# Kernel optimization log

Hardware: AMD Instinct MI355X
Metric: run time of the kernel (lower is better)

## Reference

```python
import jax, jax.numpy as jnp
import numpy as np

B, N, D, H = 4, 4096, 128, 8
DH = D // H
EPS = 1e-6


def _layernorm(x, g, b):
    mu = jnp.mean(x, axis=-1, keepdims=True)
    var = jnp.var(x, axis=-1, keepdims=True)
    return (x - mu) * jax.lax.rsqrt(var + EPS) * g + b


def setup_inputs() -> dict:
    key = jax.random.key(0)
    ks = jax.random.split(key, 12)
    p = lambda k, shape: (jax.random.normal(k, shape, jnp.float32) * 0.02)
    x = jax.random.normal(ks[0], (B, N, D), jnp.float32)
    # scale fx so the sigmoid of the N-length contraction is not fully saturated
    fx = jax.random.normal(ks[1], (B, N, D), jnp.float32) / N
    return {
        "x": x,
        "fx": fx,
        "ln1_g": jnp.ones((D,), jnp.float32),
        "ln1_b": jnp.zeros((D,), jnp.float32),
        "wq": p(ks[2], (D, D)),
        "wk": p(ks[3], (D, D)),
        "wv": p(ks[4], (D, D)),
        "wo": p(ks[5], (D, D)),
        "bo": jnp.zeros((D,), jnp.float32),
        "ln2_g": jnp.ones((D,), jnp.float32),
        "ln2_b": jnp.zeros((D,), jnp.float32),
        "w1": p(ks[6], (D, D)),
        "b1": jnp.zeros((D,), jnp.float32),
        "w2": p(ks[7], (D, D)),
        "b2": jnp.zeros((D,), jnp.float32),
    }


def reference(x, fx, ln1_g, ln1_b, wq, wk, wv, wo, bo, ln2_g, ln2_b, w1, b1, w2, b2):
    b, n, d = x.shape
    h, dh = H, d // H
    # --- pre-norm linear self-attention ---
    xn = _layernorm(x, ln1_g, ln1_b)
    def heads(w):  # [b,n,d] @ w^T -> [b,h,n,dh]
        return jnp.einsum('bnd,ed->bne', xn, w).reshape(b, n, h, dh).transpose(0, 2, 1, 3)
    q = jax.nn.softmax(heads(wq), axis=-1)   # softmax over feature dim
    k = jax.nn.softmax(heads(wk), axis=2)    # softmax over sequence dim
    v = heads(wv)
    ctx = jnp.einsum('bhnd,bhne->bhde', k, v)         # [b,h,dh,dh]
    attn = jnp.einsum('bhnd,bhde->bhne', q, ctx)       # [b,h,n,dh]
    attn = attn.transpose(0, 2, 1, 3).reshape(b, n, d)
    attn = jnp.einsum('bnd,ed->bne', attn, wo) + bo
    x = x + attn                                       # residual (dropout=identity)
    # --- pre-norm MLP ---
    y = _layernorm(x, ln2_g, ln2_b)
    y = jax.nn.gelu(jnp.einsum('bnd,ed->bne', y, w1) + b1, approximate=False)
    y = jnp.einsum('bnd,ed->bne', y, w2) + b2
    x = x + y
    # --- quadratic update: sigmoid((x x^T) fx), as written in the module ---
    gram = jnp.einsum('bnd,bmd->bnm', x, x)            # [b,n,n] materialized, faithful
    fx = jax.nn.sigmoid(jnp.einsum('bnm,bmd->bnd', gram, fx))
    return (x, fx)
```

## Files before the change

### kernel.cpp

```cpp
#include <hip/hip_runtime.h>
#include <math.h>

#define BB 4
#define NN 4096
#define DD 128
#define MM (BB*NN)

typedef __attribute__((ext_vector_type(8))) short short8;
typedef __attribute__((ext_vector_type(4))) float f32x4;

__device__ inline short f2bf(float f) {
    unsigned u = __float_as_uint(f);
    u = (u + 0x7FFFu + ((u >> 16) & 1u)) >> 16;
    return (short)u;
}
__device__ inline float bf2f(short s) {
    return __uint_as_float(((unsigned)(unsigned short)s) << 16);
}
__device__ inline short8 pack_bf8(float4 a, float4 b) {
    short8 o;
    o[0] = f2bf(a.x); o[1] = f2bf(a.y); o[2] = f2bf(a.z); o[3] = f2bf(a.w);
    o[4] = f2bf(b.x); o[5] = f2bf(b.y); o[6] = f2bf(b.z); o[7] = f2bf(b.w);
    return o;
}
__device__ inline int swzoff(int row, int col) {
    return ((row * 128 + col) * 2) ^ ((row & 7) << 4);
}

__global__ __launch_bounds__(256) void wprep(const float* __restrict__ w0, const float* __restrict__ w1,
                                             const float* __restrict__ w2, const float* __restrict__ w3,
                                             const float* __restrict__ w4, short* __restrict__ wf) {
    int m = blockIdx.x >> 3;
    int j = (blockIdx.x & 7) * 256 + threadIdx.x;
    const float* W = (m == 0) ? w0 : (m == 1) ? w1 : (m == 2) ? w2 : (m == 3) ? w3 : w4;
    int nt = j >> 8, ks = (j >> 6) & 3, l = j & 63, r = l & 15, g = l >> 4;
    const float* src = W + (size_t)(nt * 16 + r) * DD + 32 * ks + 8 * g;
    float4 a = *(const float4*)src;
    float4 b = *(const float4*)(src + 4);
    ((short8*)(wf + (size_t)m * 16384))[j] = pack_bf8(a, b);
}

__global__ __launch_bounds__(256) void lnctx(const float* __restrict__ x,
                                             const float* __restrict__ lng,
                                             const float* __restrict__ lnb,
                                             const short* __restrict__ wf,
                                             float* __restrict__ partC,
                                             float* __restrict__ pcs) {
    __shared__ float ekL[32][132];
    __shared__ float vL[32][132];
    int t = threadIdx.x;
    int block_row = blockIdx.x * 32;
    int w = t >> 6, l = t & 63, r = l & 15, g = l >> 4;
    int rh = w >> 1, nt0 = (w & 1) << 2;
    int row0 = block_row + rh * 16;

    const float* ap = x + (size_t)(row0 + r) * DD + 8 * g;
    float4 av0[4], av1[4];
    #pragma unroll
    for (int ks = 0; ks < 4; ks++) {
        av0[ks] = *(const float4*)(ap + 32 * ks);
        av1[ks] = *(const float4*)(ap + 32 * ks + 4);
    }
    float s = 0.f, ss = 0.f;
    #pragma unroll
    for (int ks = 0; ks < 4; ks++) {
        float4 a = av0[ks], b = av1[ks];
        s  += a.x + a.y + a.z + a.w + b.x + b.y + b.z + b.w;
        ss += a.x*a.x + a.y*a.y + a.z*a.z + a.w*a.w + b.x*b.x + b.y*b.y + b.z*b.z + b.w*b.w;
    }
    s  += __shfl_xor(s, 16);  s  += __shfl_xor(s, 32);
    ss += __shfl_xor(ss, 16); ss += __shfl_xor(ss, 32);
    float mu = s * (1.0f / DD);
    float var = ss * (1.0f / DD) - mu * mu;
    float rs = rsqrtf(var + 1e-6f);

    short8 af[4];
    #pragma unroll
    for (int ks = 0; ks < 4; ks++) {
        float4 g0 = *(const float4*)(lng + 32 * ks + 8 * g);
        float4 g1 = *(const float4*)(lng + 32 * ks + 8 * g + 4);
        float4 b0 = *(const float4*)(lnb + 32 * ks + 8 * g);
        float4 b1 = *(const float4*)(lnb + 32 * ks + 8 * g + 4);
        float4 n0, n1;
        n0.x = (av0[ks].x - mu) * rs * g0.x + b0.x;
        n0.y = (av0[ks].y - mu) * rs * g0.y + b0.y;
        n0.z = (av0[ks].z - mu) * rs * g0.z + b0.z;
        n0.w = (av0[ks].w - mu) * rs * g0.w + b0.w;
        n1.x = (av1[ks].x - mu) * rs * g1.x + b1.x;
        n1.y = (av1[ks].y - mu) * rs * g1.y + b1.y;
        n1.z = (av1[ks].z - mu) * rs * g1.z + b1.z;
        n1.w = (av1[ks].w - mu) * rs * g1.w + b1.w;
        af[ks] = pack_bf8(n0, n1);
    }

    f32x4 acc[2][4];
    #pragma unroll
    for (int m = 0; m < 2; m++)
        #pragma unroll
        for (int n = 0; n < 4; n++) acc[m][n] = (f32x4){0.f, 0.f, 0.f, 0.f};
    const short8* wp8 = (const short8*)wf;
    #pragma unroll
    for (int ks = 0; ks < 4; ks++)
        #pragma unroll
        for (int m = 0; m < 2; m++)
            #pragma unroll
            for (int n = 0; n < 4; n++)
                acc[m][n] = __builtin_amdgcn_mfma_f32_16x16x32_bf16(
                    af[ks], wp8[(size_t)m * 2048 + ((nt0 + n) * 4 + ks) * 64 + l], acc[m][n], 0, 0, 0);

    #pragma unroll
    for (int n = 0; n < 4; n++) {
        int col = (nt0 + n) * 16 + r;
        #pragma unroll
        for (int j = 0; j < 4; j++) {
            int rowL = rh * 16 + 4 * g + j;
            ekL[rowL][col] = __expf(acc[0][n][j]);
            vL[rowL][col]  = acc[1][n][j];
        }
    }
    __syncthreads();

    int h = t >> 5, sub = t & 31, d = sub >> 1, e0 = (sub & 1) * 8;
    float cs = 0.f;
    float sc[8] = {0.f, 0.f, 0.f, 0.f, 0.f, 0.f, 0.f, 0.f};
    #pragma unroll 8
    for (int row = 0; row < 32; row++) {
        float ekv = ekL[row][h * 16 + d];
        float4 v0 = *(const float4*)&vL[row][h * 16 + e0];
        float4 v1 = *(const float4*)&vL[row][h * 16 + e0 + 4];
        sc[0] += ekv * v0.x; sc[1] += ekv * v0.y; sc[2] += ekv * v0.z; sc[3] += ekv * v0.w;
        sc[4] += ekv * v1.x; sc[5] += ekv * v1.y; sc[6] += ekv * v1.z; sc[7] += ekv * v1.w;
        cs += ekv;
    }
    float* cb = partC + (size_t)blockIdx.x * 2048 + h * 256 + d * 16 + e0;
    *(float4*)cb       = (float4){sc[0], sc[1], sc[2], sc[3]};
    *(float4*)(cb + 4) = (float4){sc[4], sc[5], sc[6], sc[7]};
    if ((sub & 1) == 0) pcs[(size_t)blockIdx.x * 128 + h * 16 + d] = cs;
}

__global__ __launch_bounds__(256) void ctxred(const float* __restrict__ part,
                                              float* __restrict__ ctxacc) {
    int k = blockIdx.x;
    int b = k >> 4, s0 = (k & 15) * 128;
    int t = threadIdx.x;
    int slot = s0 + (t & 127), half = t >> 7;
    float s = 0.f;
    #pragma unroll 8
    for (int c = half * 64; c < half * 64 + 64; c++)
        s += part[(size_t)((b << 7) + c) * 2048 + slot];
    __shared__ float red[128];
    if (half) red[t & 127] = s;
    __syncthreads();
    if (!half) ctxacc[(size_t)b * 2048 + slot] = s + red[t & 127];
}

__global__ __launch_bounds__(256) void build_mt_k(const float* __restrict__ ctxacc,
                                                  const float* __restrict__ pcs,
                                                  const float* __restrict__ wo,
                                                  short* __restrict__ mtfrag) {
    int b = blockIdx.x >> 3, nt = blockIdx.x & 7;
    int t = threadIdx.x;
    __shared__ float ctxL[2048];
    __shared__ float csL[128];
    __shared__ float woL[2048];
    #pragma unroll
    for (int i = 0; i < 8; i++) {
        int idx = i * 256 + t;
        ctxL[idx] = ctxacc[(size_t)b * 2048 + idx];
        woL[idx]  = wo[(size_t)(nt * 16) * DD + idx];
    }
    if (t < 128) {
        float s = 0.f;
        #pragma unroll 8
        for (int c = 0; c < 128; c++) s += pcs[(size_t)(b * 128 + c) * 128 + t];
        csL[t] = s;
    }
    __syncthreads();
    int ks = (t >> 6) & 3, l = t & 63, r = l & 15, g = l >> 4;
    short8 o;
    #pragma unroll
    for (int i2 = 0; i2 < 8; i2++) {
        int k = 32 * ks + 8 * g + i2;
        float inv = 1.0f / csL[k];
        const float* wrow = woL + r * DD + (k >> 4) * 16;
        float s = 0.f;
        #pragma unroll
        for (int eo = 0; eo < 16; eo++) s += ctxL[k * 16 + eo] * wrow[eo];
        o[i2] = f2bf(s * inv);
    }
    ((short8*)(mtfrag + (size_t)b * 16384))[nt * 256 + t] = o;
}

__global__ __launch_bounds__(256) void fused_mid(const float* __restrict__ x,
                                                 const float* __restrict__ ln1g,
                                                 const float* __restrict__ ln1b,
                                                 const short* __restrict__ wqf,
                                                 const short* __restrict__ mtf,
                                                 const float* __restrict__ bo,
                                                 const float* __restrict__ ln2g,
                                                 const float* __restrict__ ln2b,
                                                 const short* __restrict__ w1f,
                                                 const float* __restrict__ b1,
                                                 const short* __restrict__ w2f,
                                                 const float* __restrict__ b2,
                                                 float* __restrict__ xfinal,
                                                 short* __restrict__ xbf) {
    __shared__ __align__(16) char ex[32 * 128 * 2];
    __shared__ float ex2f[32][132];
    __shared__ float redS[4][16], redSS[4][16];
    int t = threadIdx.x;
    int block_row = blockIdx.x * 32;
    int w = t >> 6, l = t & 63, r = l & 15, g = l >> 4;
    int rh = w >> 1, nt0 = (w & 1) << 2;
    int row0 = block_row + rh * 16;
    int rrow = rh * 16 + r;

    const float* ap = x + (size_t)(row0 + r) * DD + 8 * g;
    float4 av0[4], av1[4];
    #pragma unroll
    for (int ks = 0; ks < 4; ks++) {
        av0[ks] = *(const float4*)(ap + 32 * ks);
        av1[ks] = *(const float4*)(ap + 32 * ks + 4);
    }
    if ((w & 1) == 0) {
        #pragma unroll
        for (int ks = 0; ks < 4; ks++) {
            *(float4*)&ex2f[rrow][32 * ks + 8 * g]     = av0[ks];
            *(float4*)&ex2f[rrow][32 * ks + 8 * g + 4] = av1[ks];
        }
    }
    float s = 0.f, ss = 0.f;
    #pragma unroll
    for (int ks = 0; ks < 4; ks++) {
        float4 a = av0[ks], b = av1[ks];
        s  += a.x + a.y + a.z + a.w + b.x + b.y + b.z + b.w;
        ss += a.x*a.x + a.y*a.y + a.z*a.z + a.w*a.w + b.x*b.x + b.y*b.y + b.z*b.z + b.w*b.w;
    }
    s  += __shfl_xor(s, 16);  s  += __shfl_xor(s, 32);
    ss += __shfl_xor(ss, 16); ss += __shfl_xor(ss, 32);
    float mu1 = s * (1.0f / DD);
    float var1 = ss * (1.0f / DD) - mu1 * mu1;
    float rs1 = rsqrtf(var1 + 1e-6f);
    short8 af[4];
    #pragma unroll
    for (int ks = 0; ks < 4; ks++) {
        float4 g0 = *(const float4*)(ln1g + 32 * ks + 8 * g);
        float4 g1 = *(const float4*)(ln1g + 32 * ks + 8 * g + 4);
        float4 b0 = *(const float4*)(ln1b + 32 * ks + 8 * g);
        float4 b1v = *(const float4*)(ln1b + 32 * ks + 8 * g + 4);
        float4 n0, n1;
        n0.x = (av0[ks].x - mu1) * rs1 * g0.x + b0.x;
        n0.y = (av0[ks].y - mu1) * rs1 * g0.y + b0.y;
        n0.z = (av0[ks].z - mu1) * rs1 * g0.z + b0.z;
        n0.w = (av0[ks].w - mu1) * rs1 * g0.w + b0.w;
        n1.x = (av1[ks].x - mu1) * rs1 * g1.x + b1v.x;
        n1.y = (av1[ks].y - mu1) * rs1 * g1.y + b1v.y;
        n1.z = (av1[ks].z - mu1) * rs1 * g1.z + b1v.z;
        n1.w = (av1[ks].w - mu1) * rs1 * g1.w + b1v.w;
        af[ks] = pack_bf8(n0, n1);
    }

    const short8* qp = (const short8*)wqf;
    f32x4 accq[4];
    #pragma unroll
    for (int n = 0; n < 4; n++) accq[n] = (f32x4){0.f, 0.f, 0.f, 0.f};
    #pragma unroll
    for (int ks = 0; ks < 4; ks++)
        #pragma unroll
        for (int n = 0; n < 4; n++)
            accq[n] = __builtin_amdgcn_mfma_f32_16x16x32_bf16(
                af[ks], qp[((nt0 + n) * 4 + ks) * 64 + l], accq[n], 0, 0, 0);
    #pragma unroll
    for (int n = 0; n < 4; n++) {
        int col = (nt0 + n) * 16 + r;
        #pragma unroll
        for (int j = 0; j < 4; j++) {
            float e = __expf(accq[n][j]);
            float sm = e;
            sm += __shfl_xor(sm, 1); sm += __shfl_xor(sm, 2);
            sm += __shfl_xor(sm, 4); sm += __shfl_xor(sm, 8);
            *(short*)(ex + swzoff(rh * 16 + 4 * g + j, col)) = f2bf(e / sm);
        }
    }
    __syncthreads();

    short8 qf[4];
    #pragma unroll
    for (int ks = 0; ks < 4; ks++)
        qf[ks] = *(const short8*)(ex + swzoff(rrow, 32 * ks + 8 * g));
    float xres[4][4];
    #pragma unroll
    for (int n = 0; n < 4; n++)
        #pragma unroll
        for (int j = 0; j < 4; j++)
            xres[n][j] = ex2f[rh * 16 + 4 * g + j][(nt0 + n) * 16 + r];

    const short8* mp = (const short8*)(mtf + (size_t)(block_row >> 12) * 16384);
    f32x4 acc[4];
    #pragma unroll
    for (int n = 0; n < 4; n++) acc[n] = (f32x4){0.f, 0.f, 0.f, 0.f};
    #pragma unroll
    for (int ks = 0; ks < 4; ks++)
        #pragma unroll
        for (int n = 0; n < 4; n++)
            acc[n] = __builtin_amdgcn_mfma_f32_16x16x32_bf16(
                qf[ks], mp[((nt0 + n) * 4 + ks) * 64 + l], acc[n], 0, 0, 0);

    float vv[4][4];
    #pragma unroll
    for (int n = 0; n < 4; n++) {
        int col = (nt0 + n) * 16 + r;
        float bv = bo[col];
        #pragma unroll
        for (int j = 0; j < 4; j++)
            vv[n][j] = acc[n][j] + bv + xres[n][j];
    }

    #pragma unroll
    for (int j = 0; j < 4; j++) {
        float s1  = vv[0][j] + vv[1][j] + vv[2][j] + vv[3][j];
        float s2 = vv[0][j]*vv[0][j] + vv[1][j]*vv[1][j] + vv[2][j]*vv[2][j] + vv[3][j]*vv[3][j];
        s1 += __shfl_xor(s1, 1); s1 += __shfl_xor(s1, 2); s1 += __shfl_xor(s1, 4); s1 += __shfl_xor(s1, 8);
        s2 += __shfl_xor(s2, 1); s2 += __shfl_xor(s2, 2); s2 += __shfl_xor(s2, 4); s2 += __shfl_xor(s2, 8);
        if (r == 0) { redS[w][4 * g + j] = s1; redSS[w][4 * g + j] = s2; }
    }
    __syncthreads();
    int base = w & 2;
    #pragma unroll
    for (int j = 0; j < 4; j++) {
        int rr = 4 * g + j;
        float S  = redS[base][rr]  + redS[base + 1][rr];
        float SS = redSS[base][rr] + redSS[base + 1][rr];
        float mu = S * (1.0f / DD);
        float var = SS * (1.0f / DD) - mu * mu;
        float rs = rsqrtf(var + 1e-6f);
        int rowL = rh * 16 + rr;
        #pragma unroll
        for (int n = 0; n < 4; n++) {
            int col = (nt0 + n) * 16 + r;
            float y = (vv[n][j] - mu) * rs * ln2g[col] + ln2b[col];
            *(short*)(ex + swzoff(rowL, col)) = f2bf(y);
        }
    }
    __syncthreads();
    short8 yf[4];
    #pragma unroll
    for (int ks = 0; ks < 4; ks++)
        yf[ks] = *(const short8*)(ex + swzoff(rrow, 32 * ks + 8 * g));
    __syncthreads();
    const short8* w1p = (const short8*)w1f;
    f32x4 acc2[4];
    #pragma unroll
    for (int n = 0; n < 4; n++) acc2[n] = (f32x4){0.f, 0.f, 0.f, 0.f};
    #pragma unroll
    for (int ks = 0; ks < 4; ks++)
        #pragma unroll
        for (int n = 0; n < 4; n++)
            acc2[n] = __builtin_amdgcn_mfma_f32_16x16x32_bf16(
                yf[ks], w1p[((nt0 + n) * 4 + ks) * 64 + l], acc2[n], 0, 0, 0);
    #pragma unroll
    for (int n = 0; n < 4; n++) {
        int col = (nt0 + n) * 16 + r;
        float bv = b1[col];
        #pragma unroll
        for (int j = 0; j < 4; j++) {
            float v = acc2[n][j] + bv;
            v = 0.5f * v * (1.0f + erff(v * 0.70710678118654752f));
            *(short*)(ex + swzoff(rh * 16 + 4 * g + j, col)) = f2bf(v);
        }
    }
    __syncthreads();
    short8 hf[4];
    #pragma unroll
    for (int ks = 0; ks < 4; ks++)
        hf[ks] = *(const short8*)(ex + swzoff(rrow, 32 * ks + 8 * g));
    const short8* w2p = (const short8*)w2f;
    f32x4 acc3[4];
    #pragma unroll
    for (int n = 0; n < 4; n++) acc3[n] = (f32x4){0.f, 0.f, 0.f, 0.f};
    #pragma unroll
    for (int ks = 0; ks < 4; ks++)
        #pragma unroll
        for (int n = 0; n < 4; n++)
            acc3[n] = __builtin_amdgcn_mfma_f32_16x16x32_bf16(
                hf[ks], w2p[((nt0 + n) * 4 + ks) * 64 + l], acc3[n], 0, 0, 0);
    #pragma unroll
    for (int n = 0; n < 4; n++) {
        int col = (nt0 + n) * 16 + r;
        float bv = b2[col];
        #pragma unroll
        for (int j = 0; j < 4; j++) {
            float v = acc3[n][j] + bv + vv[n][j];
            size_t row = (size_t)(row0 + 4 * g + j);
            xfinal[row * DD + col] = v;
            xbf[row * DD + col] = f2bf(v);
        }
    }
}

__global__ __launch_bounds__(256) void sbuild_p(const short* __restrict__ xf,
                                                const float* __restrict__ fx,
                                                short* __restrict__ part) {
    int b = blockIdx.x >> 6, chunk = blockIdx.x & 63;
    int t = threadIdx.x;
    __shared__ float xs[64 * 128], fs[64 * 128];
    const short* xb = xf + ((size_t)b * NN + chunk * 64) * DD;
    const float* fb = fx + ((size_t)b * NN + chunk * 64) * DD;
    float4* xs4 = (float4*)xs; float4* fs4 = (float4*)fs;
    const short8* xg = (const short8*)xb; const float4* fg = (const float4*)fb;
    #pragma unroll
    for (int i = 0; i < 4; i++) {
        int j = i * 256 + t;
        short8 s8 = xg[j];
        float4 a = {bf2f(s8[0]), bf2f(s8[1]), bf2f(s8[2]), bf2f(s8[3])};
        float4 c = {bf2f(s8[4]), bf2f(s8[5]), bf2f(s8[6]), bf2f(s8[7])};
        xs4[2 * j] = a; xs4[2 * j + 1] = c;
    }
    #pragma unroll
    for (int i = 0; i < 8; i++) {
        int j = i * 256 + t;
        fs4[j] = fg[j];
    }
    __syncthreads();
    int td = t >> 4, te = t & 15;
    float acc[8][8];
    #pragma unroll
    for (int a = 0; a < 8; a++)
        #pragma unroll
        for (int c = 0; c < 8; c++) acc[a][c] = 0.f;
    for (int r = 0; r < 64; r++) {
        float4 x0 = xs4[r * 32 + td * 2], x1 = xs4[r * 32 + td * 2 + 1];
        float4 f0 = fs4[r * 32 + te * 2], f1 = fs4[r * 32 + te * 2 + 1];
        float xv[8] = {x0.x, x0.y, x0.z, x0.w, x1.x, x1.y, x1.z, x1.w};
        float fv[8] = {f0.x, f0.y, f0.z, f0.w, f1.x, f1.y, f1.z, f1.w};
        #pragma unroll
        for (int a = 0; a < 8; a++)
            #pragma unroll
            for (int c = 0; c < 8; c++) acc[a][c] = fmaf(xv[a], fv[c], acc[a][c]);
    }
    short* pb = part + (size_t)blockIdx.x * 16384;
    int d0 = td * 8, e0 = te * 8;
    #pragma unroll
    for (int ei = 0; ei < 8; ei++) {
        short8 o;
        #pragma unroll
        for (int i = 0; i < 8; i++) o[i] = f2bf(acc[i][ei]);
        *(short8*)(pb + (size_t)(e0 + ei) * DD + d0) = o;
    }
}

__global__ __launch_bounds__(256) void sreduce(const short* __restrict__ part,
                                               short* __restrict__ stfrag) {
    int b = blockIdx.x >> 6, grp = blockIdx.x & 63;
    int t = threadIdx.x;
    int slotL = t >> 3, sub = t & 7;
    int j = grp * 32 + slotL;
    int nt = j >> 8, ks = (j >> 6) & 3, l = j & 63, r = l & 15, g = l >> 4;
    int c = nt * 16 + r, k0 = 32 * ks + 8 * g;
    const short* pb = part + (size_t)b * 64 * 16384 + (size_t)c * DD + k0;
    float s[8] = {0.f, 0.f, 0.f, 0.f, 0.f, 0.f, 0.f, 0.f};
    for (int ch = sub; ch < 64; ch += 8) {
        short8 u = *(const short8*)(pb + (size_t)ch * 16384);
        #pragma unroll
        for (int i = 0; i < 8; i++) s[i] += bf2f(u[i]);
    }
    #pragma unroll
    for (int o = 1; o <= 4; o <<= 1)
        #pragma unroll
        for (int i = 0; i < 8; i++) s[i] += __shfl_xor(s[i], o);
    if (sub == 0) {
        short8 o;
        #pragma unroll
        for (int i = 0; i < 8; i++) o[i] = f2bf(s[i]);
        ((short8*)(stfrag + (size_t)b * 16384))[j] = o;
    }
}

__global__ __launch_bounds__(256) void gemm_sig(const short* __restrict__ A,
                                                const short* __restrict__ wfrag,
                                                float* __restrict__ Cf) {
    int t = threadIdx.x;
    int block_row = blockIdx.x * 32;
    int w = t >> 6, l = t & 63, r = l & 15, g = l >> 4;
    int row0 = block_row + ((w >> 1) << 4);
    int nt0 = (w & 1) << 2;
    const short8* ap = (const short8*)(A + (size_t)(row0 + r) * DD + 8 * g);
    short8 af[4];
    #pragma unroll
    for (int ks = 0; ks < 4; ks++) af[ks] = ap[ks * 4];
    const short8* wp8 = (const short8*)(wfrag + (size_t)(block_row >> 12) * 16384);
    f32x4 acc[4];
    #pragma unroll
    for (int n = 0; n < 4; n++) acc[n] = (f32x4){0.f, 0.f, 0.f, 0.f};
    #pragma unroll
    for (int ks = 0; ks < 4; ks++)
        #pragma unroll
        for (int n = 0; n < 4; n++)
            acc[n] = __builtin_amdgcn_mfma_f32_16x16x32_bf16(
                af[ks], wp8[((nt0 + n) * 4 + ks) * 64 + l], acc[n], 0, 0, 0);
    #pragma unroll
    for (int n = 0; n < 4; n++) {
        int col = (nt0 + n) * 16 + r;
        #pragma unroll
        for (int j = 0; j < 4; j++) {
            float v = 1.0f / (1.0f + __expf(-acc[n][j]));
            Cf[(size_t)(row0 + 4 * g + j) * DD + col] = v;
        }
    }
}

extern "C" void kernel_launch(void* const* d_in, const int* in_sizes, int n_in,
                              void* d_out, int out_size, void* d_ws, size_t ws_size,
                              hipStream_t stream) {
    const float* x    = (const float*)d_in[0];
    const float* fx   = (const float*)d_in[1];
    const float* ln1g = (const float*)d_in[2];
    const float* ln1b = (const float*)d_in[3];
    const float* wq   = (const float*)d_in[4];
    const float* wk   = (const float*)d_in[5];
    const float* wv   = (const float*)d_in[6];
    const float* wo   = (const float*)d_in[7];
    const float* bo   = (const float*)d_in[8];
    const float* ln2g = (const float*)d_in[9];
    const float* ln2b = (const float*)d_in[10];
    const float* w1   = (const float*)d_in[11];
    const float* b1   = (const float*)d_in[12];
    const float* w2   = (const float*)d_in[13];
    const float* b2   = (const float*)d_in[14];

    float* out = (float*)d_out;
    float* xfinal = out;
    float* fxout  = out + (size_t)MM * DD;

    float* ws = (float*)d_ws;
    short* xbf    = (short*)ws;
    short* partSb = (short*)(ws + 1048576);
    short* wfW    = (short*)(ws + 3145728);
    float* partC  = ws + 3145728 + 40960;
    float* pcs    = partC + 1048576;
    float* ctxacc = pcs + 65536;
    short* mtf    = (short*)(ctxacc + 8192);
    short* stf    = mtf + 65536;

    wprep<<<40, 256, 0, stream>>>(wq, wk, wv, w1, w2, wfW);
    lnctx<<<512, 256, 0, stream>>>(x, ln1g, ln1b, wfW + 16384, partC, pcs);
    ctxred<<<64, 256, 0, stream>>>(partC, ctxacc);
    build_mt_k<<<32, 256, 0, stream>>>(ctxacc, pcs, wo, mtf);
    fused_mid<<<512, 256, 0, stream>>>(x, ln1g, ln1b, wfW, mtf, bo, ln2g, ln2b,
                                       wfW + 3 * 16384, b1, wfW + 4 * 16384, b2,
                                       xfinal, xbf);
    sbuild_p<<<256, 256, 0, stream>>>(xbf, fx, partSb);
    sreduce<<<256, 256, 0, stream>>>(partSb, stf);
    gemm_sig<<<512, 256, 0, stream>>>(xbf, stf, fxout);
}
```

Measured before the change: 74.47 us.

## Fold ctx reduction into build_mt, widen sbuild_p, simplify S reduction layout

Removes the ctxred kernel by having each build_mt_k block sum the 128 per-chunk context partials itself. sbuild_p now runs with 512 threads and smaller per-thread tiles. The fragment-ordered bf16 S reduction is replaced with a plain fp32 S_T reduction, and gemm_sig converts it to bf16 MFMA fragments on load. The aim is to save one launch and increase parallelism. In exchange, build_mt_k now does redundant serial reduction work, since 8 blocks per batch each reread the same 1 MB of partials with only 32 blocks in the grid. gemm_sig also does redundant fp32 loads and conversions.

```diff
diff --git a/kernel.cpp b/kernel.cpp
--- a/kernel.cpp
+++ b/kernel.cpp
@@ -138,23 +138,7 @@
     if ((sub & 1) == 0) pcs[(size_t)blockIdx.x * 128 + h * 16 + d] = cs;
 }
 
-__global__ __launch_bounds__(256) void ctxred(const float* __restrict__ part,
-                                              float* __restrict__ ctxacc) {
-    int k = blockIdx.x;
-    int b = k >> 4, s0 = (k & 15) * 128;
-    int t = threadIdx.x;
-    int slot = s0 + (t & 127), half = t >> 7;
-    float s = 0.f;
-    #pragma unroll 8
-    for (int c = half * 64; c < half * 64 + 64; c++)
-        s += part[(size_t)((b << 7) + c) * 2048 + slot];
-    __shared__ float red[128];
-    if (half) red[t & 127] = s;
-    __syncthreads();
-    if (!half) ctxacc[(size_t)b * 2048 + slot] = s + red[t & 127];
-}
-
-__global__ __launch_bounds__(256) void build_mt_k(const float* __restrict__ ctxacc,
+__global__ __launch_bounds__(256) void build_mt_k(const float* __restrict__ partC,
                                                   const float* __restrict__ pcs,
                                                   const float* __restrict__ wo,
                                                   short* __restrict__ mtfrag) {
@@ -163,11 +147,20 @@
     __shared__ float ctxL[2048];
     __shared__ float csL[128];
     __shared__ float woL[2048];
+    {
+        float s[8] = {0.f,0.f,0.f,0.f,0.f,0.f,0.f,0.f};
+        for (int c = 0; c < 128; c++) {
+            const float* pp = partC + (size_t)(b * 128 + c) * 2048 + t;
+            #pragma unroll
+            for (int i = 0; i < 8; i++) s[i] += pp[i * 256];
+        }
+        #pragma unroll
+        for (int i = 0; i < 8; i++) ctxL[i * 256 + t] = s[i];
+    }
     #pragma unroll
     for (int i = 0; i < 8; i++) {
         int idx = i * 256 + t;
-        ctxL[idx] = ctxacc[(size_t)b * 2048 + idx];
-        woL[idx]  = wo[(size_t)(nt * 16) * DD + idx];
+        woL[idx] = wo[(size_t)(nt * 16) * DD + idx];
     }
     if (t < 128) {
         float s = 0.f;
@@ -398,7 +391,7 @@
     }
 }
 
-__global__ __launch_bounds__(256) void sbuild_p(const short* __restrict__ xf,
+__global__ __launch_bounds__(512) void sbuild_p(const short* __restrict__ xf,
                                                 const float* __restrict__ fx,
                                                 short* __restrict__ part) {
     int b = blockIdx.x >> 6, chunk = blockIdx.x & 63;
@@ -406,78 +399,66 @@
     __shared__ float xs[64 * 128], fs[64 * 128];
     const short* xb = xf + ((size_t)b * NN + chunk * 64) * DD;
     const float* fb = fx + ((size_t)b * NN + chunk * 64) * DD;
+    const short8* xg = (const short8*)xb;
     float4* xs4 = (float4*)xs; float4* fs4 = (float4*)fs;
-    const short8* xg = (const short8*)xb; const float4* fg = (const float4*)fb;
-    #pragma unroll
-    for (int i = 0; i < 4; i++) {
-        int j = i * 256 + t;
+    const float4* fg = (const float4*)fb;
+    #pragma unroll
+    for (int i = 0; i < 2; i++) {
+        int j = i * 512 + t;
         short8 s8 = xg[j];
         float4 a = {bf2f(s8[0]), bf2f(s8[1]), bf2f(s8[2]), bf2f(s8[3])};
         float4 c = {bf2f(s8[4]), bf2f(s8[5]), bf2f(s8[6]), bf2f(s8[7])};
         xs4[2 * j] = a; xs4[2 * j + 1] = c;
     }
     #pragma unroll
-    for (int i = 0; i < 8; i++) {
-        int j = i * 256 + t;
+    for (int i = 0; i < 4; i++) {
+        int j = i * 512 + t;
         fs4[j] = fg[j];
     }
     __syncthreads();
-    int td = t >> 4, te = t & 15;
-    float acc[8][8];
+    int td = t & 15, te = t >> 4;
+    float acc[8][4];
     #pragma unroll
     for (int a = 0; a < 8; a++)
         #pragma unroll
-        for (int c = 0; c < 8; c++) acc[a][c] = 0.f;
+        for (int c = 0; c < 4; c++) acc[a][c] = 0.f;
     for (int r = 0; r < 64; r++) {
         float4 x0 = xs4[r * 32 + td * 2], x1 = xs4[r * 32 + td * 2 + 1];
-        float4 f0 = fs4[r * 32 + te * 2], f1 = fs4[r * 32 + te * 2 + 1];
+        float4 f0 = fs4[r * 32 + te];
         float xv[8] = {x0.x, x0.y, x0.z, x0.w, x1.x, x1.y, x1.z, x1.w};
-        float fv[8] = {f0.x, f0.y, f0.z, f0.w, f1.x, f1.y, f1.z, f1.w};
+        float fv[4] = {f0.x, f0.y, f0.z, f0.w};
         #pragma unroll
         for (int a = 0; a < 8; a++)
             #pragma unroll
-            for (int c = 0; c < 8; c++) acc[a][c] = fmaf(xv[a], fv[c], acc[a][c]);
+            for (int c = 0; c < 4; c++) acc[a][c] = fmaf(xv[a], fv[c], acc[a][c]);
     }
     short* pb = part + (size_t)blockIdx.x * 16384;
-    int d0 = td * 8, e0 = te * 8;
-    #pragma unroll
-    for (int ei = 0; ei < 8; ei++) {
+    #pragma unroll
+    for (int ci = 0; ci < 4; ci++) {
         short8 o;
         #pragma unroll
-        for (int i = 0; i < 8; i++) o[i] = f2bf(acc[i][ei]);
-        *(short8*)(pb + (size_t)(e0 + ei) * DD + d0) = o;
-    }
-}
-
-__global__ __launch_bounds__(256) void sreduce(const short* __restrict__ part,
-                                               short* __restrict__ stfrag) {
-    int b = blockIdx.x >> 6, grp = blockIdx.x & 63;
+        for (int a = 0; a < 8; a++) o[a] = f2bf(acc[a][ci]);
+        *(short8*)(pb + (size_t)(te * 4 + ci) * 128 + td * 8) = o;
+    }
+}
+
+__global__ __launch_bounds__(256) void sreduce2(const short* __restrict__ part,
+                                                float* __restrict__ S_T) {
+    int b = blockIdx.x >> 7, e = blockIdx.x & 127;
     int t = threadIdx.x;
-    int slotL = t >> 3, sub = t & 7;
-    int j = grp * 32 + slotL;
-    int nt = j >> 8, ks = (j >> 6) & 3, l = j & 63, r = l & 15, g = l >> 4;
-    int c = nt * 16 + r, k0 = 32 * ks + 8 * g;
-    const short* pb = part + (size_t)b * 64 * 16384 + (size_t)c * DD + k0;
-    float s[8] = {0.f, 0.f, 0.f, 0.f, 0.f, 0.f, 0.f, 0.f};
-    for (int ch = sub; ch < 64; ch += 8) {
-        short8 u = *(const short8*)(pb + (size_t)ch * 16384);
-        #pragma unroll
-        for (int i = 0; i < 8; i++) s[i] += bf2f(u[i]);
-    }
-    #pragma unroll
-    for (int o = 1; o <= 4; o <<= 1)
-        #pragma unroll
-        for (int i = 0; i < 8; i++) s[i] += __shfl_xor(s[i], o);
-    if (sub == 0) {
-        short8 o;
-        #pragma unroll
-        for (int i = 0; i < 8; i++) o[i] = f2bf(s[i]);
-        ((short8*)(stfrag + (size_t)b * 16384))[j] = o;
-    }
+    int d = t & 127, half = t >> 7;
+    float s = 0.f;
+    #pragma unroll 4
+    for (int ch = half * 32; ch < half * 32 + 32; ch++)
+        s += bf2f(part[(size_t)(b * 64 + ch) * 16384 + e * 128 + d]);
+    __shared__ float red[128];
+    if (half) red[d] = s;
+    __syncthreads();
+    if (!half) S_T[((size_t)b * 128 + e) * 128 + d] = s + red[d];
 }
 
 __global__ __launch_bounds__(256) void gemm_sig(const short* __restrict__ A,
-                                                const short* __restrict__ wfrag,
+                                                const float* __restrict__ S_T,
                                                 float* __restrict__ Cf) {
     int t = threadIdx.x;
     int block_row = blockIdx.x * 32;
@@ -488,7 +469,18 @@
     short8 af[4];
     #pragma unroll
     for (int ks = 0; ks < 4; ks++) af[ks] = ap[ks * 4];
-    const short8* wp8 = (const short8*)(wfrag + (size_t)(block_row >> 12) * 16384);
+    const float* sp = S_T + (size_t)(block_row >> 12) * 16384;
+    short8 bf[4][4];
+    #pragma unroll
+    for (int n = 0; n < 4; n++) {
+        const float* se = sp + (size_t)((nt0 + n) * 16 + r) * 128 + 8 * g;
+        #pragma unroll
+        for (int ks = 0; ks < 4; ks++) {
+            float4 a = *(const float4*)(se + 32 * ks);
+            float4 c = *(const float4*)(se + 32 * ks + 4);
+            bf[n][ks] = pack_bf8(a, c);
+        }
+    }
     f32x4 acc[4];
     #pragma unroll
     for (int n = 0; n < 4; n++) acc[n] = (f32x4){0.f, 0.f, 0.f, 0.f};
@@ -497,7 +489,7 @@
         #pragma unroll
         for (int n = 0; n < 4; n++)
             acc[n] = __builtin_amdgcn_mfma_f32_16x16x32_bf16(
-                af[ks], wp8[((nt0 + n) * 4 + ks) * 64 + l], acc[n], 0, 0, 0);
+                af[ks], bf[n][ks], acc[n], 0, 0, 0);
     #pragma unroll
     for (int n = 0; n < 4; n++) {
         int col = (nt0 + n) * 16 + r;
@@ -538,18 +530,16 @@
     short* wfW    = (short*)(ws + 3145728);
     float* partC  = ws + 3145728 + 40960;
     float* pcs    = partC + 1048576;
-    float* ctxacc = pcs + 65536;
-    short* mtf    = (short*)(ctxacc + 8192);
-    short* stf    = mtf + 65536;
+    float* S_T    = pcs + 65536;
+    short* mtf    = (short*)(S_T + 65536);
 
     wprep<<<40, 256, 0, stream>>>(wq, wk, wv, w1, w2, wfW);
     lnctx<<<512, 256, 0, stream>>>(x, ln1g, ln1b, wfW + 16384, partC, pcs);
-    ctxred<<<64, 256, 0, stream>>>(partC, ctxacc);
-    build_mt_k<<<32, 256, 0, stream>>>(ctxacc, pcs, wo, mtf);
+    build_mt_k<<<32, 256, 0, stream>>>(partC, pcs, wo, mtf);
     fused_mid<<<512, 256, 0, stream>>>(x, ln1g, ln1b, wfW, mtf, bo, ln2g, ln2b,
                                        wfW + 3 * 16384, b1, wfW + 4 * 16384, b2,
                                        xfinal, xbf);
-    sbuild_p<<<256, 256, 0, stream>>>(xbf, fx, partSb);
-    sreduce<<<256, 256, 0, stream>>>(partSb, stf);
-    gemm_sig<<<512, 256, 0, stream>>>(xbf, stf, fxout);
-}
+    sbuild_p<<<256, 512, 0, stream>>>(xbf, fx, partSb);
+    sreduce2<<<512, 256, 0, stream>>>(partSb, S_T);
+    gemm_sig<<<512, 256, 0, stream>>>(xbf, S_T, fxout);
+}
```

New measurement: 84.37 us. 13.3% more time.
